# Performance work log

Measured on AMD Instinct MI355X. Metric: run time of the kernel, lower is better.

## Reference

```python
import jax, jax.numpy as jnp
import numpy as np
from jax import lax

BIT_SIZE = 8
ES_SIZE = 1


def posit_quantize(x, nbits=BIT_SIZE, es=ES_SIZE):
    """Round x to the nearest posit(nbits, es) representable value (round-to-nearest
    of the fraction given the regime/exponent-dependent fraction width)."""
    sign = jnp.sign(x)
    a = jnp.abs(x)
    safe = jnp.where(a > 0, a, jnp.ones_like(a))
    logx = jnp.floor(jnp.log2(safe))            # binade exponent
    ipow = 2 ** es                               # 2^es, python int
    k = jnp.floor(logx / ipow)                   # regime value
    regime_len = jnp.where(k >= 0, k + 2, -k + 1)
    fbits = jnp.clip(nbits - 1 - regime_len - es, 0, 23)  # fraction bits left
    scale = jnp.exp2(logx)
    frac = safe / scale                          # in [1, 2)
    step = jnp.exp2(fbits)
    q = jnp.round(frac * step) / step * scale
    maxpos = jnp.float32(2.0 ** ((nbits - 2) * ipow))
    minpos = jnp.float32(2.0 ** (-(nbits - 2) * ipow))
    q = jnp.clip(q, minpos, maxpos)
    return jnp.where(a > 0, sign * q, jnp.zeros_like(x))


def pq(x):
    # straight-through quantizer (forward value is exact posit rounding)
    return x + lax.stop_gradient(posit_quantize(x) - x)


def conv2d(x, w):  # NCHW, OIHW, valid, stride 1
    return lax.conv_general_dilated(x, w, (1, 1), 'VALID',
                                    dimension_numbers=('NCHW', 'OIHW', 'NCHW'))


def maxpool2(x):
    return lax.reduce_window(x, -jnp.inf, lax.max,
                             (1, 1, 2, 2), (1, 1, 2, 2), 'VALID')


def setup_inputs() -> dict:
    key = jax.random.key(0)
    ks = jax.random.split(key, 9)
    B = 4096
    x = jax.random.normal(ks[0], (B, 1, 28, 28), jnp.float32)
    def init_w(k, shape, fan_in):
        bound = 1.0 / np.sqrt(fan_in)
        return jax.random.uniform(k, shape, jnp.float32, -bound, bound)
    conv1_w = init_w(ks[1], (32, 1, 3, 3), 1 * 9)
    conv1_b = init_w(ks[2], (32,), 1 * 9)
    conv2_w = init_w(ks[3], (64, 32, 3, 3), 32 * 9)
    conv2_b = init_w(ks[4], (64,), 32 * 9)
    fc1_w = init_w(ks[5], (128, 12 * 12 * 64), 12 * 12 * 64)
    fc1_b = init_w(ks[6], (128,), 12 * 12 * 64)
    fc2_w = init_w(ks[7], (10, 128), 128)
    fc2_b = init_w(ks[8], (10,), 128)
    return dict(x=x, conv1_w=conv1_w, conv1_b=conv1_b, conv2_w=conv2_w,
                conv2_b=conv2_b, fc1_w=fc1_w, fc1_b=fc1_b,
                fc2_w=fc2_w, fc2_b=fc2_b)


def reference(x, conv1_w, conv1_b, conv2_w, conv2_b, fc1_w, fc1_b, fc2_w, fc2_b):
    # PositizedConv2d: posit-quantize activations and weights, conv in fp32, add bias
    h = conv2d(pq(x), pq(conv1_w)) + conv1_b[None, :, None, None]   # [B,32,26,26]
    h = jax.nn.relu(h)
    h = conv2d(pq(h), pq(conv2_w)) + conv2_b[None, :, None, None]   # [B,64,24,24]
    h = jax.nn.relu(h)
    h = maxpool2(h)                                                  # [B,64,12,12]
    # dropout layers are identity in eval mode
    h = h.reshape(-1, 12 * 12 * 64)
    h = jax.nn.relu(jnp.dot(pq(h), pq(fc1_w).T) + fc1_b)             # [B,128]
    out = jnp.dot(pq(h), pq(fc2_w).T) + fc2_b                        # [B,10]
    return out
```

## Files before the change

kernel.cpp:

```cpp
#include <hip/hip_runtime.h>

using u16 = unsigned short;
using u32 = unsigned int;
typedef __attribute__((ext_vector_type(8))) short bf16x8;
typedef __attribute__((ext_vector_type(4))) float f32x4;

__device__ __forceinline__ float posit_q(float x) {
    float a = __builtin_fabsf(x);
    u32 u = __float_as_uint(a);
    int logx = (int)(u >> 23) - 127;
    logx = logx < -60 ? -60 : (logx > 60 ? 60 : logx);
    float frac = __uint_as_float((u & 0x007fffffu) | 0x3f800000u);
    int k = logx >> 1;
    int rl = (k >= 0) ? (k + 2) : (1 - k);
    int fb = 6 - rl; fb = fb < 0 ? 0 : fb;
    float step = (float)(1 << fb);
    float q = rintf(frac * step) * __uint_as_float((u32)(127 + logx - fb) << 23);
    q = fminf(fmaxf(q, 0x1p-12f), 0x1p12f);
    return (a > 0.0f) ? copysignf(q, x) : 0.0f;
}

__device__ __forceinline__ float b2f(u16 v) { return __uint_as_float((u32)v << 16); }
__device__ __forceinline__ u16 f2b(float f) { return (u16)(__float_as_uint(f) >> 16); }

__device__ __forceinline__ void lut_init(int tid, float* lut) {
    if (tid < 256) {
        int e = tid - 127;
        float m = 0.f;
        if (e >= -12 && e <= 12) {
            int k = e >> 1;
            int rl = max(k + 2, 1 - k);
            int fb = max(6 - rl, 0);
            m = __uint_as_float((u32)(150 + e - fb) << 23) * 1.5f;
        }
        lut[tid] = m;
    }
}
__device__ __forceinline__ u32 pq_pos_raw(float x, const float* __restrict__ lut) {
    u32 u = __float_as_uint(x);
    float c = lut[u >> 23];
    float q = (x + c) - c;
    q = fminf(fmaxf(q, 0x1p-12f), 0x1p12f);
    return u == 0u ? 0u : __float_as_uint(q);
}

__global__ __launch_bounds__(256) void prep_kernel(
    const float* __restrict__ w1, const float* __restrict__ w2,
    const float* __restrict__ fw2,
    float* __restrict__ w1q, u16* __restrict__ w2frag, float* __restrict__ fc2wq) {
    int i = blockIdx.x * 256 + threadIdx.x;
    if (i < 288)  w1q[i]   = posit_q(w1[i]);
    if (i < 1280) fc2wq[i] = posit_q(fw2[i]);
    if (i < 18432) {
        int e = i & 7, lane = (i >> 3) & 63, c9 = i >> 9;
        int kc = c9 % 9, nt = c9 / 9;
        int n = nt * 16 + (lane & 15);
        int ci = ((lane >> 4) << 3) + e;
        w2frag[i] = f2b(posit_q(w2[n * 288 + ci * 9 + kc]));
    }
}

#define PLS 5416
__global__ __launch_bounds__(512, 4) void conv_fused_kernel(
    const float* __restrict__ x, const float* __restrict__ w1q, const float* __restrict__ b1,
    const u16* __restrict__ w2frag, const float* __restrict__ b2,
    const float* __restrict__ fw1, u16* __restrict__ fc1wq, u16* __restrict__ pooled) {
    __shared__ __align__(16) float sX[784];
    __shared__ __align__(16) u16 sH1[4 * PLS];
    __shared__ __align__(16) u16 sPool[64 * 152];
    __shared__ float sLut[256];
    int img = blockIdx.x, tid = threadIdx.x;
    int wave = tid >> 6, lane = tid & 63;
    int col = lane & 15, quad = lane >> 4;

    lut_init(tid, sLut);

    for (int i = tid; i < 784; i += 512) sX[i] = posit_q(x[(size_t)img * 784 + i]);
    if (tid < 288) fc1wq[(size_t)img * 288 + tid] = f2b(posit_q(fw1[(size_t)img * 288 + tid]));

    int ocp = tid & 15;
    float wreg[18];
#pragma unroll
    for (int j = 0; j < 18; ++j) wreg[j] = w1q[ocp * 18 + j];
    float bias0 = b1[ocp * 2], bias1 = b1[ocp * 2 + 1];

    __syncthreads();

    int pgrp = tid >> 4;
    u16* h1dst = &sH1[(ocp >> 2) * PLS + 2 * (ocp & 3)];
    for (int it = 0; it < 22; ++it) {
        int p = it * 32 + pgrp;
        if (p < 676) {
            int y = p / 26, xx = p - y * 26;
            const float* px = &sX[y * 28 + xx];
            float in9[9];
#pragma unroll
            for (int r = 0; r < 3; ++r)
#pragma unroll
                for (int c = 0; c < 3; ++c) in9[r * 3 + c] = px[r * 28 + c];
            float a0 = bias0, a1 = bias1;
#pragma unroll
            for (int j = 0; j < 9; ++j) {
                a0 = fmaf(wreg[j], in9[j], a0);
                a1 = fmaf(wreg[9 + j], in9[j], a1);
            }
            u32 r0 = pq_pos_raw(fmaxf(a0, 0.f), sLut);
            u32 r1 = pq_pos_raw(fmaxf(a1, 0.f), sLut);
            *(u32*)&h1dst[p * 8] = (r0 >> 16) | (r1 & 0xFFFF0000u);
        }
    }

    __syncthreads();
    int npair = wave & 1, mq = wave >> 1;
    bf16x8 bfrag[2][9];
#pragma unroll
    for (int j = 0; j < 2; ++j)
#pragma unroll
        for (int kc = 0; kc < 9; ++kc)
            bfrag[j][kc] = *(const bf16x8*)(w2frag + (((npair * 2 + j) * 9 + kc) * 64 + lane) * 8);
    float cb0 = b2[(npair * 2) * 16 + col];
    float cb1 = b2[(npair * 2 + 1) * 16 + col];
    int poolb0 = ((npair * 2) * 16 + col) * 152;
    int poolb1 = ((npair * 2 + 1) * 16 + col) * 152;
    const u16* aplane = &sH1[quad * PLS];

    for (int t = 0; t < 9; ++t) {
        int mt = mq * 9 + t;
        int m = mt * 16 + col;
        int pp = m >> 2, wi = m & 3;
        int py = pp / 12, px_ = pp - py * 12;
        int oh = 2 * py + (wi >> 1), ow = 2 * px_ + (wi & 1);
        const u16* ap = aplane + (oh * 26 + ow) * 8;
        f32x4 acc0 = {0.f, 0.f, 0.f, 0.f}, acc1 = {0.f, 0.f, 0.f, 0.f};
#pragma unroll
        for (int kc = 0; kc < 9; ++kc) {
            int kh = kc / 3, kw = kc - kh * 3;
            bf16x8 af = *(const bf16x8*)(ap + (kh * 26 + kw) * 8);
            acc0 = __builtin_amdgcn_mfma_f32_16x16x32_bf16(af, bfrag[0][kc], acc0, 0, 0, 0);
            acc1 = __builtin_amdgcn_mfma_f32_16x16x32_bf16(af, bfrag[1][kc], acc1, 0, 0, 0);
        }
        float mx0 = fmaxf(fmaxf(acc0[0], acc0[1]), fmaxf(acc0[2], acc0[3]));
        float mx1 = fmaxf(fmaxf(acc1[0], acc1[1]), fmaxf(acc1[2], acc1[3]));
        sPool[poolb0 + mt * 4 + quad] = (u16)(pq_pos_raw(fmaxf(mx0 + cb0, 0.f), sLut) >> 16);
        sPool[poolb1 + mt * 4 + quad] = (u16)(pq_pos_raw(fmaxf(mx1 + cb1, 0.f), sLut) >> 16);
    }
    __syncthreads();

    for (int u = tid; u < 1152; u += 512) {
        int c = u / 18, g = u - c * 18;
        uint4 v = *(const uint4*)&sPool[c * 152 + g * 8];
        *(uint4*)(pooled + (size_t)img * 9216 + c * 144 + g * 8) = v;
    }
}

__global__ __launch_bounds__(512, 2) void fc_kernel(const u16* __restrict__ pooled,
    const u16* __restrict__ fc1wq, const float* __restrict__ fc1b,
    const float* __restrict__ fc2wq, const float* __restrict__ fc2b,
    float* __restrict__ out) {
    __shared__ __align__(16) float sAcc[4][16 * 132];
    __shared__ __align__(16) u16 sFc1[16 * 128];
    __shared__ float sW2[1280];
    __shared__ float sB2[16];
    __shared__ float sLut[256];
    int blk = blockIdx.x, tid = threadIdx.x;
    int wave = tid >> 6, lane = tid & 63;
    int row = lane & 15, quad = lane >> 4;
    int m0 = blk * 16;
    lut_init(tid, sLut);
    for (int i = tid; i < 1280; i += 512) sW2[i] = fc2wq[i];
    if (tid < 10) sB2[tid] = fc2b[tid];

    const bf16x8* ap = (const bf16x8*)(pooled + (size_t)(m0 + row) * 9216 + wave * 1152) + quad;
    const bf16x8* bp[8];
#pragma unroll
    for (int nt = 0; nt < 8; ++nt)
        bp[nt] = (const bf16x8*)(fc1wq + (size_t)(nt * 16 + row) * 9216 + wave * 1152) + quad;
    f32x4 acc[8];
#pragma unroll
    for (int nt = 0; nt < 8; ++nt) acc[nt] = f32x4{0.f, 0.f, 0.f, 0.f};
#pragma unroll 4
    for (int ks = 0; ks < 36; ++ks) {
        bf16x8 a = ap[ks * 4];
#pragma unroll
        for (int nt = 0; nt < 8; ++nt)
            acc[nt] = __builtin_amdgcn_mfma_f32_16x16x32_bf16(a, bp[nt][ks * 4], acc[nt], 0, 0, 0);
    }
    if (wave < 4) {
#pragma unroll
        for (int nt = 0; nt < 8; ++nt)
#pragma unroll
            for (int r = 0; r < 4; ++r)
                sAcc[wave][(quad * 4 + r) * 132 + nt * 16 + row] = acc[nt][r];
    }
    __syncthreads();
    if (wave >= 4) {
#pragma unroll
        for (int nt = 0; nt < 8; ++nt)
#pragma unroll
            for (int r = 0; r < 4; ++r)
                sAcc[wave - 4][(quad * 4 + r) * 132 + nt * 16 + row] += acc[nt][r];
    }
    __syncthreads();
    for (int e = tid; e < 2048; e += 512) {
        int ml = e >> 7, n = e & 127;
        int o = ml * 132 + n;
        float s = sAcc[0][o] + sAcc[1][o] + sAcc[2][o] + sAcc[3][o];
        sFc1[e] = (u16)(pq_pos_raw(fmaxf(s + fc1b[n], 0.f), sLut) >> 16);
    }
    __syncthreads();
    if (tid < 160) {
        int il = tid / 10, oc = tid - il * 10;
        float s = sB2[oc];
        const u16* hp = &sFc1[il * 128];
        const float* wp = &sW2[oc * 128];
#pragma unroll
        for (int k = 0; k < 128; ++k) s = fmaf(b2f(hp[k]), wp[k], s);
        out[(size_t)(m0 + il) * 10 + oc] = s;
    }
}

extern "C" void kernel_launch(void* const* d_in, const int* in_sizes, int n_in,
                              void* d_out, int out_size, void* d_ws, size_t ws_size,
                              hipStream_t stream) {
    const float* x    = (const float*)d_in[0];
    const float* w1   = (const float*)d_in[1];
    const float* b1   = (const float*)d_in[2];
    const float* w2   = (const float*)d_in[3];
    const float* b2   = (const float*)d_in[4];
    const float* fw1  = (const float*)d_in[5];
    const float* fb1  = (const float*)d_in[6];
    const float* fw2  = (const float*)d_in[7];
    const float* fb2  = (const float*)d_in[8];
    float* out = (float*)d_out;

    char* ws = (char*)d_ws;
    float* w1q     = (float*)(ws + 0);
    float* fc2wq   = (float*)(ws + 1280);
    u16*   w2frag  = (u16*)(ws + 6400);
    u16*   fc1wq   = (u16*)(ws + 43520);
    u16*   pooled  = (u16*)(ws + 2402816);

    prep_kernel<<<72, 256, 0, stream>>>(w1, w2, fw2, w1q, w2frag, fc2wq);
    conv_fused_kernel<<<4096, 512, 0, stream>>>(x, w1q, b1, w2frag, b2, fw1, fc1wq, pooled);
    fc_kernel<<<256, 512, 0, stream>>>(pooled, fc1wq, fb1, fc2wq, fb2, out);
}
```

Before: 270.5 us.

## Double conv block size and split fc1 over K into partial-sum kernels

Raises the conv kernel to 1024 threads per block (16 waves), halving conv1 loop iterations and splitting the conv2 M-tiles 5/4 per wave group. Splits the fc1 GEMM four ways over K across 1024 blocks that write fp32 partials, then adds a reduce kernel that sums them, applies bias, relu, posit rounding and fc2. This aims to fill the GPU better in the fc stage, which had only 256 blocks. The cost is an extra launch and partial-sum traffic to and from global memory. The 1024-thread conv block with launch bounds asking for 8 blocks may force heavy register pressure or spills.

After: 613.3 us. +126.7%, slower.

```diff
diff --git a/kernel.cpp b/kernel.cpp
--- a/kernel.cpp
+++ b/kernel.cpp
@@ -61,7 +61,7 @@
 }
 
 #define PLS 5416
-__global__ __launch_bounds__(512, 4) void conv_fused_kernel(
+__global__ __launch_bounds__(1024, 8) void conv_fused_kernel(
     const float* __restrict__ x, const float* __restrict__ w1q, const float* __restrict__ b1,
     const u16* __restrict__ w2frag, const float* __restrict__ b2,
     const float* __restrict__ fw1, u16* __restrict__ fc1wq, u16* __restrict__ pooled) {
@@ -75,7 +75,7 @@
 
     lut_init(tid, sLut);
 
-    for (int i = tid; i < 784; i += 512) sX[i] = posit_q(x[(size_t)img * 784 + i]);
+    for (int i = tid; i < 784; i += 1024) sX[i] = posit_q(x[(size_t)img * 784 + i]);
     if (tid < 288) fc1wq[(size_t)img * 288 + tid] = f2b(posit_q(fw1[(size_t)img * 288 + tid]));
 
     int ocp = tid & 15;
@@ -88,8 +88,8 @@
 
     int pgrp = tid >> 4;
     u16* h1dst = &sH1[(ocp >> 2) * PLS + 2 * (ocp & 3)];
-    for (int it = 0; it < 22; ++it) {
-        int p = it * 32 + pgrp;
+    for (int it = 0; it < 11; ++it) {
+        int p = it * 64 + pgrp;
         if (p < 676) {
             int y = p / 26, xx = p - y * 26;
             const float* px = &sX[y * 28 + xx];
@@ -112,6 +112,8 @@
 
     __syncthreads();
     int npair = wave & 1, mq = wave >> 1;
+    int tcnt = (mq < 4) ? 5 : 4;
+    int tstart = (mq < 4) ? mq * 5 : 20 + (mq - 4) * 4;
     bf16x8 bfrag[2][9];
 #pragma unroll
     for (int j = 0; j < 2; ++j)
@@ -124,8 +126,8 @@
     int poolb1 = ((npair * 2 + 1) * 16 + col) * 152;
     const u16* aplane = &sH1[quad * PLS];
 
-    for (int t = 0; t < 9; ++t) {
-        int mt = mq * 9 + t;
+    for (int t = 0; t < tcnt; ++t) {
+        int mt = tstart + t;
         int m = mt * 16 + col;
         int pp = m >> 2, wi = m & 3;
         int py = pp / 12, px_ = pp - py * 12;
@@ -146,66 +148,75 @@
     }
     __syncthreads();
 
-    for (int u = tid; u < 1152; u += 512) {
+    for (int u = tid; u < 1152; u += 1024) {
         int c = u / 18, g = u - c * 18;
         uint4 v = *(const uint4*)&sPool[c * 152 + g * 8];
         *(uint4*)(pooled + (size_t)img * 9216 + c * 144 + g * 8) = v;
     }
 }
 
-__global__ __launch_bounds__(512, 2) void fc_kernel(const u16* __restrict__ pooled,
-    const u16* __restrict__ fc1wq, const float* __restrict__ fc1b,
-    const float* __restrict__ fc2wq, const float* __restrict__ fc2b,
-    float* __restrict__ out) {
+__global__ __launch_bounds__(512, 8) void fc1_part_kernel(const u16* __restrict__ pooled,
+    const u16* __restrict__ fc1wq, float* __restrict__ part) {
     __shared__ __align__(16) float sAcc[4][16 * 132];
-    __shared__ __align__(16) u16 sFc1[16 * 128];
+    int blk = blockIdx.x, tid = threadIdx.x;
+    int mb = blk >> 2, ks = blk & 3;
+    int wave = tid >> 6, lane = tid & 63;
+    int row = lane & 15, quad = lane >> 4;
+    size_t kbase = (size_t)ks * 2304 + wave * 288;
+
+    const bf16x8* ap = (const bf16x8*)(pooled + (size_t)(mb * 16 + row) * 9216 + kbase) + quad;
+    const bf16x8* bp[8];
+#pragma unroll
+    for (int nt = 0; nt < 8; ++nt)
+        bp[nt] = (const bf16x8*)(fc1wq + (size_t)(nt * 16 + row) * 9216 + kbase) + quad;
+    f32x4 acc[8];
+#pragma unroll
+    for (int nt = 0; nt < 8; ++nt) acc[nt] = f32x4{0.f, 0.f, 0.f, 0.f};
+#pragma unroll 3
+    for (int k2 = 0; k2 < 9; ++k2) {
+        bf16x8 a = ap[k2 * 4];
+#pragma unroll
+        for (int nt = 0; nt < 8; ++nt)
+            acc[nt] = __builtin_amdgcn_mfma_f32_16x16x32_bf16(a, bp[nt][k2 * 4], acc[nt], 0, 0, 0);
+    }
+    if (wave < 4) {
+#pragma unroll
+        for (int nt = 0; nt < 8; ++nt)
+#pragma unroll
+            for (int r = 0; r < 4; ++r)
+                sAcc[wave][(quad * 4 + r) * 132 + nt * 16 + row] = acc[nt][r];
+    }
+    __syncthreads();
+    if (wave >= 4) {
+#pragma unroll
+        for (int nt = 0; nt < 8; ++nt)
+#pragma unroll
+            for (int r = 0; r < 4; ++r)
+                sAcc[wave - 4][(quad * 4 + r) * 132 + nt * 16 + row] += acc[nt][r];
+    }
+    __syncthreads();
+    for (int e = tid; e < 2048; e += 512) {
+        int o = (e >> 7) * 132 + (e & 127);
+        part[(size_t)blk * 2048 + e] = sAcc[0][o] + sAcc[1][o] + sAcc[2][o] + sAcc[3][o];
+    }
+}
+
+__global__ __launch_bounds__(256) void fc2_red_kernel(const float* __restrict__ part,
+    const float* __restrict__ fc1b, const float* __restrict__ fc2wq,
+    const float* __restrict__ fc2b, float* __restrict__ out) {
+    __shared__ __align__(16) u16 sFc1[2048];
     __shared__ float sW2[1280];
     __shared__ float sB2[16];
     __shared__ float sLut[256];
-    int blk = blockIdx.x, tid = threadIdx.x;
-    int wave = tid >> 6, lane = tid & 63;
-    int row = lane & 15, quad = lane >> 4;
-    int m0 = blk * 16;
+    int mb = blockIdx.x, tid = threadIdx.x;
     lut_init(tid, sLut);
-    for (int i = tid; i < 1280; i += 512) sW2[i] = fc2wq[i];
+    for (int i = tid; i < 1280; i += 256) sW2[i] = fc2wq[i];
     if (tid < 10) sB2[tid] = fc2b[tid];
-
-    const bf16x8* ap = (const bf16x8*)(pooled + (size_t)(m0 + row) * 9216 + wave * 1152) + quad;
-    const bf16x8* bp[8];
-#pragma unroll
-    for (int nt = 0; nt < 8; ++nt)
-        bp[nt] = (const bf16x8*)(fc1wq + (size_t)(nt * 16 + row) * 9216 + wave * 1152) + quad;
-    f32x4 acc[8];
-#pragma unroll
-    for (int nt = 0; nt < 8; ++nt) acc[nt] = f32x4{0.f, 0.f, 0.f, 0.f};
-#pragma unroll 4
-    for (int ks = 0; ks < 36; ++ks) {
-        bf16x8 a = ap[ks * 4];
-#pragma unroll
-        for (int nt = 0; nt < 8; ++nt)
-            acc[nt] = __builtin_amdgcn_mfma_f32_16x16x32_bf16(a, bp[nt][ks * 4], acc[nt], 0, 0, 0);
-    }
-    if (wave < 4) {
-#pragma unroll
-        for (int nt = 0; nt < 8; ++nt)
-#pragma unroll
-            for (int r = 0; r < 4; ++r)
-                sAcc[wave][(quad * 4 + r) * 132 + nt * 16 + row] = acc[nt][r];
-    }
-    __syncthreads();
-    if (wave >= 4) {
-#pragma unroll
-        for (int nt = 0; nt < 8; ++nt)
-#pragma unroll
-            for (int r = 0; r < 4; ++r)
-                sAcc[wave - 4][(quad * 4 + r) * 132 + nt * 16 + row] += acc[nt][r];
-    }
-    __syncthreads();
-    for (int e = tid; e < 2048; e += 512) {
-        int ml = e >> 7, n = e & 127;
-        int o = ml * 132 + n;
-        float s = sAcc[0][o] + sAcc[1][o] + sAcc[2][o] + sAcc[3][o];
-        sFc1[e] = (u16)(pq_pos_raw(fmaxf(s + fc1b[n], 0.f), sLut) >> 16);
+    __syncthreads();
+    const float* pb = part + (size_t)mb * 4 * 2048;
+    for (int e = tid; e < 2048; e += 256) {
+        float s = pb[e] + pb[2048 + e] + pb[4096 + e] + pb[6144 + e];
+        sFc1[e] = (u16)(pq_pos_raw(fmaxf(s + fc1b[e & 127], 0.f), sLut) >> 16);
     }
     __syncthreads();
     if (tid < 160) {
@@ -215,7 +226,7 @@
         const float* wp = &sW2[oc * 128];
 #pragma unroll
         for (int k = 0; k < 128; ++k) s = fmaf(b2f(hp[k]), wp[k], s);
-        out[(size_t)(m0 + il) * 10 + oc] = s;
+        out[(size_t)(mb * 16 + il) * 10 + oc] = s;
     }
 }
 
@@ -239,8 +250,10 @@
     u16*   w2frag  = (u16*)(ws + 6400);
     u16*   fc1wq   = (u16*)(ws + 43520);
     u16*   pooled  = (u16*)(ws + 2402816);
+    float* part    = (float*)(ws + 77900288);
 
     prep_kernel<<<72, 256, 0, stream>>>(w1, w2, fw2, w1q, w2frag, fc2wq);
-    conv_fused_kernel<<<4096, 512, 0, stream>>>(x, w1q, b1, w2frag, b2, fw1, fc1wq, pooled);
-    fc_kernel<<<256, 512, 0, stream>>>(pooled, fc1wq, fb1, fc2wq, fb2, out);
-}
+    conv_fused_kernel<<<4096, 1024, 0, stream>>>(x, w1q, b1, w2frag, b2, fw1, fc1wq, pooled);
+    fc1_part_kernel<<<1024, 512, 0, stream>>>(pooled, fc1wq, part);
+    fc2_red_kernel<<<256, 256, 0, stream>>>(part, fb1, fc2wq, fb2, out);
+}
```
